# Kernel tuning notes

Hardware: AMD Instinct MI355X
Metric: run time of the kernel (lower is better)

## Reference

```python
import jax, jax.numpy as jnp
import numpy as np

N_NODES = 100000
N_EDGES = 600000
IN_FEAT = 128
OUT_FEAT = 128
NUM_RELS = 8
NUM_BASES = 4


def setup_inputs() -> dict:
    key = jax.random.key(0)
    ks = jax.random.split(key, 8)
    h = jax.random.normal(ks[0], (N_NODES, IN_FEAT), dtype=jnp.float32)
    # xavier-ish scale for params
    weight = jax.random.normal(ks[1], (NUM_BASES, IN_FEAT, OUT_FEAT), dtype=jnp.float32) * (1.0 / np.sqrt(IN_FEAT))
    w_comp = jax.random.normal(ks[2], (NUM_RELS, NUM_BASES), dtype=jnp.float32) * (1.0 / np.sqrt(NUM_BASES))
    root_weight = jax.random.normal(ks[3], (IN_FEAT, OUT_FEAT), dtype=jnp.float32) * (1.0 / np.sqrt(IN_FEAT))
    bias = jnp.zeros((OUT_FEAT,), dtype=jnp.float32)
    src = jax.random.randint(ks[4], (N_EDGES,), 0, N_NODES, dtype=jnp.int32)
    dst = jax.random.randint(ks[5], (N_EDGES,), 0, N_NODES, dtype=jnp.int32)
    rel_type = jax.random.randint(ks[6], (N_EDGES,), 0, NUM_RELS, dtype=jnp.int32)
    return {"h": h, "weight": weight, "w_comp": w_comp, "root_weight": root_weight,
            "bias": bias, "src": src, "dst": dst, "rel_type": rel_type}


def reference(h, weight, w_comp, root_weight, bias, src, dst, rel_type):
    # Basis decomposition: W[r] = sum_b w_comp[r,b] * weight[b]
    B, I, O = weight.shape
    R = w_comp.shape[0]
    W = (w_comp @ weight.reshape(B, I * O)).reshape(R, I, O)  # [R, in, out]
    # msg_e = h[src_e] @ W[rel_e]; computed as all-relation projection + gather
    # (avoids materializing [E, in, out] per-edge weights)
    proj = jnp.einsum('ni,rio->nro', h, W)          # [N, R, out]
    msg = proj[src, rel_type]                        # [E, out]
    agg = jax.ops.segment_sum(msg, dst, num_segments=h.shape[0])  # scatter-sum
    out = h @ root_weight + agg + bias
    return jax.nn.relu(out)
```

## Files before the change

kernel.cpp:

```cpp
#include <hip/hip_runtime.h>
#include <hip/hip_bf16.h>

#define N_NODES 100000
#define N_EDGES 600000
#define FEAT 128
#define NUM_RELS 8
#define NUM_BASES 4
#define NBE 2344

#define PREP_CAST 6250
#define PREP_BLDB 320
#define PREP_ZERO 392
#define PREP_GRID (PREP_CAST + PREP_BLDB + PREP_ZERO)

#define SCAN_TILES 98

typedef short bf16x8 __attribute__((ext_vector_type(8)));
typedef float f32x4  __attribute__((ext_vector_type(4)));
typedef float f32x2  __attribute__((ext_vector_type(2)));

__device__ inline short f2bf(float x) {
    __hip_bfloat16 b = __float2bfloat16(x);
    return *reinterpret_cast<short*>(&b);
}
__device__ inline float bfbits2f(unsigned int u16) {
    return __int_as_float(u16 << 16);
}


__global__ __launch_bounds__(256) void k_prep(const float* __restrict__ h,
                                              const float* __restrict__ weight,
                                              const float* __restrict__ rw,
                                              short* __restrict__ hb,
                                              short* __restrict__ Bt,
                                              int* __restrict__ cnt,
                                              int* __restrict__ status) {
    int b = blockIdx.x;
    if (b < PREP_CAST) {
        int i = b * 256 + threadIdx.x;
        const float4* h4 = (const float4*)h;
        float4 v0 = h4[2 * i], v1 = h4[2 * i + 1];
        union { short s[8]; bf16x8 v; } u;
        u.s[0] = f2bf(v0.x); u.s[1] = f2bf(v0.y); u.s[2] = f2bf(v0.z); u.s[3] = f2bf(v0.w);
        u.s[4] = f2bf(v1.x); u.s[5] = f2bf(v1.y); u.s[6] = f2bf(v1.z); u.s[7] = f2bf(v1.w);
        ((bf16x8*)hb)[i] = u.v;
    } else if (b < PREP_CAST + PREP_BLDB) {
        int idx = (b - PREP_CAST) * 256 + threadIdx.x;
        int kc = idx >> 14;
        int e  = idx & 16383;
        int o  = e >> 7, ip = e & 127;
        float v = (kc == 0) ? rw[ip * FEAT + o]
                            : weight[(kc - 1) * FEAT * FEAT + ip * FEAT + o];
        Bt[idx] = f2bf(v);
    } else {
        int i = (b - PREP_CAST - PREP_BLDB) * 256 + threadIdx.x;
        if (i < N_NODES) cnt[i] = 0;
        else if (i - N_NODES < 128) status[i - N_NODES] = 0;
    }
}

__global__ __launch_bounds__(256) void k_hist_dst(const int* __restrict__ dst,
                                                  int* __restrict__ cnt) {
    int i = blockIdx.x * 256 + threadIdx.x;
    if (i < N_EDGES) atomicAdd(&cnt[dst[i]], 1);
}

__global__ __launch_bounds__(256) void k_scan_lb(const int* __restrict__ cnt,
                                                 int* __restrict__ offs,
                                                 int* __restrict__ cursor,
                                                 int* __restrict__ status) {
    __shared__ int wsum[4];
    __shared__ int bcast;
    int bid = blockIdx.x;
    int lane = threadIdx.x & 63, wid = threadIdx.x >> 6;
    const int N4 = N_NODES / 4;
    int i4 = bid * 256 + threadIdx.x;

    const int4* cnt4 = (const int4*)cnt;
    int4 v = (i4 < N4) ? cnt4[i4] : make_int4(0, 0, 0, 0);
    int s = v.x + v.y + v.z + v.w;
    int incl = s;
#pragma unroll
    for (int d = 1; d < 64; d <<= 1) {
        int t = __shfl_up(incl, d);
        if (lane >= d) incl += t;
    }
    if (lane == 63) wsum[wid] = incl;
    __syncthreads();
    if (threadIdx.x == 0) {
        int a = 0;
#pragma unroll
        for (int w = 0; w < 4; ++w) { int x = wsum[w]; wsum[w] = a; a += x; }
        int total = a;
        __hip_atomic_store(&status[bid], (total << 2) | 1,
                           __ATOMIC_RELEASE, __HIP_MEMORY_SCOPE_AGENT);
        int excl = 0;
        for (int t = bid - 1; t >= 0; ) {
            int st = __hip_atomic_load(&status[t],
                                       __ATOMIC_ACQUIRE, __HIP_MEMORY_SCOPE_AGENT);
            if ((st & 3) == 0) { __builtin_amdgcn_s_sleep(1); continue; }
            excl += st >> 2;
            if ((st & 3) == 2) break;
            --t;
        }
        __hip_atomic_store(&status[bid], ((excl + total) << 2) | 2,
                           __ATOMIC_RELEASE, __HIP_MEMORY_SCOPE_AGENT);
        bcast = excl;
        if (bid == SCAN_TILES - 1) offs[N_NODES] = excl + total;
    }
    __syncthreads();
    int base = bcast + wsum[wid] + incl - s;
    if (i4 < N4) {
        int4 ex;
        ex.x = base;
        ex.y = base + v.x;
        ex.z = base + v.x + v.y;
        ex.w = base + v.x + v.y + v.z;
        ((int4*)offs)[i4]   = ex;
        ((int4*)cursor)[i4] = ex;
    }
}

__global__ __launch_bounds__(256) void k_scatter_sorted(const int* __restrict__ src,
                                                        const int* __restrict__ dst,
                                                        const int* __restrict__ rel,
                                                        const float* __restrict__ wc,
                                                        int* __restrict__ cursor,
                                                        int* __restrict__ srcs,
                                                        float4* __restrict__ coef) {
    int e = blockIdx.x * 256 + threadIdx.x;
    if (e < N_EDGES) {
        int p = atomicAdd(&cursor[dst[e]], 1);
        srcs[p] = src[e];
        int r = rel[e] * NUM_BASES;
        coef[p] = make_float4(wc[r], wc[r + 1], wc[r + 2], wc[r + 3]);
    }
}

__global__ __launch_bounds__(256) void k_edge_z(const int* __restrict__ offs,
                                                const int* __restrict__ srcs,
                                                const float4* __restrict__ coef,
                                                const short* __restrict__ hb,
                                                unsigned int* __restrict__ z_u32) {
    int wid = threadIdx.x >> 6, lane = threadIdx.x & 63;
    int d = blockIdx.x * 4 + wid;
    if (d >= N_NODES) return;
    int s = offs[d], e = offs[d + 1];

    f32x2 z2[4] = {(f32x2)0.f, (f32x2)0.f, (f32x2)0.f, (f32x2)0.f};

    int i = s;
    for (; i + 1 < e; i += 2) {
        int s0 = srcs[i], s1 = srcs[i + 1];
        float4 c0 = coef[i], c1 = coef[i + 1];
        unsigned int v0 = ((const unsigned int*)(hb + (size_t)s0 * FEAT))[lane];
        unsigned int v1 = ((const unsigned int*)(hb + (size_t)s1 * FEAT))[lane];
        f32x2 h0; h0.x = bfbits2f(v0 & 0xffffu); h0.y = bfbits2f(v0 >> 16);
        f32x2 h1; h1.x = bfbits2f(v1 & 0xffffu); h1.y = bfbits2f(v1 >> 16);
        f32x2 cc;
        cc = c0.x; z2[0] += cc * h0;
        cc = c0.y; z2[1] += cc * h0;
        cc = c0.z; z2[2] += cc * h0;
        cc = c0.w; z2[3] += cc * h0;
        cc = c1.x; z2[0] += cc * h1;
        cc = c1.y; z2[1] += cc * h1;
        cc = c1.z; z2[2] += cc * h1;
        cc = c1.w; z2[3] += cc * h1;
    }
    if (i < e) {
        int s0 = srcs[i];
        float4 c0 = coef[i];
        unsigned int v0 = ((const unsigned int*)(hb + (size_t)s0 * FEAT))[lane];
        f32x2 h0; h0.x = bfbits2f(v0 & 0xffffu); h0.y = bfbits2f(v0 >> 16);
        f32x2 cc;
        cc = c0.x; z2[0] += cc * h0;
        cc = c0.y; z2[1] += cc * h0;
        cc = c0.z; z2[2] += cc * h0;
        cc = c0.w; z2[3] += cc * h0;
    }

    unsigned int* row = z_u32 + (size_t)d * 256;
#pragma unroll
    for (int b = 0; b < 4; ++b) {
        unsigned int lo = ((unsigned int)(unsigned short)f2bf(z2[b].x));
        unsigned int hi = ((unsigned int)(unsigned short)f2bf(z2[b].y)) << 16;
        row[b * 64 + lane] = lo | hi;
    }
}

__global__ __launch_bounds__(256) void k_gemm_fused(const short* __restrict__ hb,
                                                    const short* __restrict__ z,
                                                    const short* __restrict__ Bt,
                                                    const float* __restrict__ bias,
                                                    float* __restrict__ out) {
    __shared__ short lds[FEAT * FEAT];
    int wave = threadIdx.x >> 6, lane = threadIdx.x & 63;
    int quad = lane >> 4, n16 = lane & 15;
    int base = blockIdx.x * 128 + wave * 32;

    int rowA0 = base + n16;        if (rowA0 >= N_NODES) rowA0 = N_NODES - 1;
    int rowA1 = base + 16 + n16;   if (rowA1 >= N_NODES) rowA1 = N_NODES - 1;

    f32x4 acc[2][8];
#pragma unroll
    for (int mt = 0; mt < 2; ++mt)
#pragma unroll
        for (int nt = 0; nt < 8; ++nt) acc[mt][nt] = (f32x4)0.f;

    float4* l4 = (float4*)lds;
    const bf16x8* bp = (const bf16x8*)lds;

    for (int kc = 0; kc < 5; ++kc) {
        if (kc) __syncthreads();
        const float4* s4 = (const float4*)(Bt + kc * FEAT * FEAT);
#pragma unroll
        for (int t = 0; t < 8; ++t) {
            int linear = threadIdx.x + t * 256;
            int o = linear >> 4, c = linear & 15;
            l4[(o << 4) + ((c + (o >> 3)) & 15)] = s4[linear];
        }
        __syncthreads();

        const bf16x8* a0p = (kc == 0)
            ? (const bf16x8*)(hb + (size_t)rowA0 * FEAT)
            : (const bf16x8*)(z + (size_t)rowA0 * 512 + (kc - 1) * FEAT);
        const bf16x8* a1p = (kc == 0)
            ? (const bf16x8*)(hb + (size_t)rowA1 * FEAT)
            : (const bf16x8*)(z + (size_t)rowA1 * 512 + (kc - 1) * FEAT);

#pragma unroll
        for (int ks = 0; ks < 4; ++ks) {
            bf16x8 a0 = a0p[ks * 4 + quad];
            bf16x8 a1 = a1p[ks * 4 + quad];
            int sw = (ks * 4 + quad + n16) & 15;
#pragma unroll
            for (int nt = 0; nt < 8; ++nt) {
                int o = n16 * 8 + nt;
                bf16x8 b = bp[(o << 4) + sw];
                acc[0][nt] = __builtin_amdgcn_mfma_f32_16x16x32_bf16(a0, b, acc[0][nt], 0, 0, 0);
                acc[1][nt] = __builtin_amdgcn_mfma_f32_16x16x32_bf16(a1, b, acc[1][nt], 0, 0, 0);
            }
        }
    }

    float bv[8];
#pragma unroll
    for (int nt = 0; nt < 8; ++nt) bv[nt] = bias[n16 * 8 + nt];

#pragma unroll
    for (int mt = 0; mt < 2; ++mt)
#pragma unroll
        for (int reg = 0; reg < 4; ++reg) {
            int node = base + mt * 16 + quad * 4 + reg;
            if (node < N_NODES) {
                float4 fa, fb;
                fa.x = fmaxf(acc[mt][0][reg] + bv[0], 0.f);
                fa.y = fmaxf(acc[mt][1][reg] + bv[1], 0.f);
                fa.z = fmaxf(acc[mt][2][reg] + bv[2], 0.f);
                fa.w = fmaxf(acc[mt][3][reg] + bv[3], 0.f);
                fb.x = fmaxf(acc[mt][4][reg] + bv[4], 0.f);
                fb.y = fmaxf(acc[mt][5][reg] + bv[5], 0.f);
                fb.z = fmaxf(acc[mt][6][reg] + bv[6], 0.f);
                fb.w = fmaxf(acc[mt][7][reg] + bv[7], 0.f);
                float* row = out + (size_t)node * FEAT + n16 * 8;
                *(float4*)row       = fa;
                *(float4*)(row + 4) = fb;
            }
        }
}


extern "C" void kernel_launch(void* const* d_in, const int* in_sizes, int n_in,
                              void* d_out, int out_size, void* d_ws, size_t ws_size,
                              hipStream_t stream) {
    const float* h    = (const float*)d_in[0];
    const float* wgt  = (const float*)d_in[1];
    const float* wcmp = (const float*)d_in[2];
    const float* rw   = (const float*)d_in[3];
    const float* bias = (const float*)d_in[4];
    const int*   src  = (const int*)d_in[5];
    const int*   dst  = (const int*)d_in[6];
    const int*   rel  = (const int*)d_in[7];
    float* out = (float*)d_out;

    char* ws = (char*)d_ws;
    short*        hb     = (short*)(ws + 0);
    short*        Bt     = (short*)(ws + 25600000ull);
    short*        z      = (short*)(ws + 25763840ull);
    unsigned int* z_u32  = (unsigned int*)z;
    int*          srcs   = (int*)(ws + 128163840ull);
    float4*       coef   = (float4*)(ws + 130563840ull);
    int*          cnt    = (int*)(ws + 140163840ull);
    int*          offs   = (int*)(ws + 140563840ull);
    int*          cursor = (int*)(ws + 140963968ull);
    int*          status = (int*)(ws + 141363968ull);

    hipLaunchKernelGGL(k_prep,     dim3(PREP_GRID), dim3(256), 0, stream,
                       h, wgt, rw, hb, Bt, cnt, status);
    hipLaunchKernelGGL(k_hist_dst, dim3(NBE),  dim3(256), 0, stream, dst, cnt);
    hipLaunchKernelGGL(k_scan_lb,  dim3(SCAN_TILES), dim3(256), 0, stream,
                       cnt, offs, cursor, status);
    hipLaunchKernelGGL(k_scatter_sorted, dim3(NBE), dim3(256), 0, stream,
                       src, dst, rel, wcmp, cursor, srcs, coef);
    hipLaunchKernelGGL(k_edge_z,   dim3((N_NODES + 3) / 4), dim3(256), 0, stream,
                       offs, srcs, coef, hb, z_u32);
    hipLaunchKernelGGL(k_gemm_fused, dim3((N_NODES + 127) / 128), dim3(256), 0, stream,
                       hb, z, Bt, bias, out);
}
```

Before: 285.6 us.

## Pack src and relation into one int and broadcast edge data via readlane

The scatter kernel now writes a single packed int per edge (src shifted left by 3, OR relation) instead of a src int plus a float4 of basis coefficients, so it writes 4 bytes per edge instead of 20. The edge kernel loads up to 64 packed entries at once, one per lane, and broadcasts each with readlane instead of every lane loading the same srcs and coef entries. Basis coefficients come from a tiny table in shared memory indexed by relation. This adds a block-wide barrier and LDS lookups, and relies on src fitting in 29 bits.

```diff
diff --git a/kernel.cpp b/kernel.cpp
--- a/kernel.cpp
+++ b/kernel.cpp
@@ -124,24 +124,27 @@
 __global__ __launch_bounds__(256) void k_scatter_sorted(const int* __restrict__ src,
                                                         const int* __restrict__ dst,
                                                         const int* __restrict__ rel,
-                                                        const float* __restrict__ wc,
                                                         int* __restrict__ cursor,
-                                                        int* __restrict__ srcs,
-                                                        float4* __restrict__ coef) {
+                                                        int* __restrict__ packed) {
     int e = blockIdx.x * 256 + threadIdx.x;
     if (e < N_EDGES) {
         int p = atomicAdd(&cursor[dst[e]], 1);
-        srcs[p] = src[e];
-        int r = rel[e] * NUM_BASES;
-        coef[p] = make_float4(wc[r], wc[r + 1], wc[r + 2], wc[r + 3]);
+        packed[p] = (src[e] << 3) | rel[e];
     }
 }
 
 __global__ __launch_bounds__(256) void k_edge_z(const int* __restrict__ offs,
-                                                const int* __restrict__ srcs,
-                                                const float4* __restrict__ coef,
+                                                const int* __restrict__ packed,
+                                                const float* __restrict__ wc,
                                                 const short* __restrict__ hb,
                                                 unsigned int* __restrict__ z_u32) {
+    __shared__ float4 wcs[NUM_RELS];
+    if (threadIdx.x < NUM_RELS) {
+        int r = threadIdx.x * NUM_BASES;
+        wcs[threadIdx.x] = make_float4(wc[r], wc[r + 1], wc[r + 2], wc[r + 3]);
+    }
+    __syncthreads();
+
     int wid = threadIdx.x >> 6, lane = threadIdx.x & 63;
     int d = blockIdx.x * 4 + wid;
     if (d >= N_NODES) return;
@@ -149,34 +152,43 @@
 
     f32x2 z2[4] = {(f32x2)0.f, (f32x2)0.f, (f32x2)0.f, (f32x2)0.f};
 
-    int i = s;
-    for (; i + 1 < e; i += 2) {
-        int s0 = srcs[i], s1 = srcs[i + 1];
-        float4 c0 = coef[i], c1 = coef[i + 1];
-        unsigned int v0 = ((const unsigned int*)(hb + (size_t)s0 * FEAT))[lane];
-        unsigned int v1 = ((const unsigned int*)(hb + (size_t)s1 * FEAT))[lane];
-        f32x2 h0; h0.x = bfbits2f(v0 & 0xffffu); h0.y = bfbits2f(v0 >> 16);
-        f32x2 h1; h1.x = bfbits2f(v1 & 0xffffu); h1.y = bfbits2f(v1 >> 16);
-        f32x2 cc;
-        cc = c0.x; z2[0] += cc * h0;
-        cc = c0.y; z2[1] += cc * h0;
-        cc = c0.z; z2[2] += cc * h0;
-        cc = c0.w; z2[3] += cc * h0;
-        cc = c1.x; z2[0] += cc * h1;
-        cc = c1.y; z2[1] += cc * h1;
-        cc = c1.z; z2[2] += cc * h1;
-        cc = c1.w; z2[3] += cc * h1;
-    }
-    if (i < e) {
-        int s0 = srcs[i];
-        float4 c0 = coef[i];
-        unsigned int v0 = ((const unsigned int*)(hb + (size_t)s0 * FEAT))[lane];
-        f32x2 h0; h0.x = bfbits2f(v0 & 0xffffu); h0.y = bfbits2f(v0 >> 16);
-        f32x2 cc;
-        cc = c0.x; z2[0] += cc * h0;
-        cc = c0.y; z2[1] += cc * h0;
-        cc = c0.z; z2[2] += cc * h0;
-        cc = c0.w; z2[3] += cc * h0;
+    for (int base = s; base < e; base += 64) {
+        int rem = e - base;
+        int m = rem < 64 ? rem : 64;
+        int pk = (lane < m) ? packed[base + lane] : 0;
+        int j = 0;
+        for (; j + 1 < m; j += 2) {
+            int p0 = __builtin_amdgcn_readlane(pk, j);
+            int p1 = __builtin_amdgcn_readlane(pk, j + 1);
+            int s0 = p0 >> 3, s1 = p1 >> 3;
+            float4 c0 = wcs[p0 & 7];
+            float4 c1 = wcs[p1 & 7];
+            unsigned int v0 = ((const unsigned int*)(hb + (size_t)s0 * FEAT))[lane];
+            unsigned int v1 = ((const unsigned int*)(hb + (size_t)s1 * FEAT))[lane];
+            f32x2 h0; h0.x = bfbits2f(v0 & 0xffffu); h0.y = bfbits2f(v0 >> 16);
+            f32x2 h1; h1.x = bfbits2f(v1 & 0xffffu); h1.y = bfbits2f(v1 >> 16);
+            f32x2 cc;
+            cc = c0.x; z2[0] += cc * h0;
+            cc = c0.y; z2[1] += cc * h0;
+            cc = c0.z; z2[2] += cc * h0;
+            cc = c0.w; z2[3] += cc * h0;
+            cc = c1.x; z2[0] += cc * h1;
+            cc = c1.y; z2[1] += cc * h1;
+            cc = c1.z; z2[2] += cc * h1;
+            cc = c1.w; z2[3] += cc * h1;
+        }
+        if (j < m) {
+            int p0 = __builtin_amdgcn_readlane(pk, j);
+            int s0 = p0 >> 3;
+            float4 c0 = wcs[p0 & 7];
+            unsigned int v0 = ((const unsigned int*)(hb + (size_t)s0 * FEAT))[lane];
+            f32x2 h0; h0.x = bfbits2f(v0 & 0xffffu); h0.y = bfbits2f(v0 >> 16);
+            f32x2 cc;
+            cc = c0.x; z2[0] += cc * h0;
+            cc = c0.y; z2[1] += cc * h0;
+            cc = c0.z; z2[2] += cc * h0;
+            cc = c0.w; z2[3] += cc * h0;
+        }
     }
 
     unsigned int* row = z_u32 + (size_t)d * 256;
@@ -288,12 +300,11 @@
     short*        Bt     = (short*)(ws + 25600000ull);
     short*        z      = (short*)(ws + 25763840ull);
     unsigned int* z_u32  = (unsigned int*)z;
-    int*          srcs   = (int*)(ws + 128163840ull);
-    float4*       coef   = (float4*)(ws + 130563840ull);
-    int*          cnt    = (int*)(ws + 140163840ull);
-    int*          offs   = (int*)(ws + 140563840ull);
-    int*          cursor = (int*)(ws + 140963968ull);
-    int*          status = (int*)(ws + 141363968ull);
+    int*          packed = (int*)(ws + 128163840ull);
+    int*          cnt    = (int*)(ws + 130563840ull);
+    int*          offs   = (int*)(ws + 130963840ull);
+    int*          cursor = (int*)(ws + 131363968ull);
+    int*          status = (int*)(ws + 131763968ull);
 
     hipLaunchKernelGGL(k_prep,     dim3(PREP_GRID), dim3(256), 0, stream,
                        h, wgt, rw, hb, Bt, cnt, status);
@@ -301,9 +312,9 @@
     hipLaunchKernelGGL(k_scan_lb,  dim3(SCAN_TILES), dim3(256), 0, stream,
                        cnt, offs, cursor, status);
     hipLaunchKernelGGL(k_scatter_sorted, dim3(NBE), dim3(256), 0, stream,
-                       src, dst, rel, wcmp, cursor, srcs, coef);
+                       src, dst, rel, cursor, packed);
     hipLaunchKernelGGL(k_edge_z,   dim3((N_NODES + 3) / 4), dim3(256), 0, stream,
-                       offs, srcs, coef, hb, z_u32);
+                       offs, packed, wcmp, hb, z_u32);
     hipLaunchKernelGGL(k_gemm_fused, dim3((N_NODES + 127) / 128), dim3(256), 0, stream,
                        hb, z, Bt, bias, out);
 }
```

Result: faster. 276.9 us (-3.0%).
